# Kernel tuning notes

Hardware: AMD Instinct MI355X
Metric: run time of the kernel (lower is better)

## Reference

```python
import jax, jax.numpy as jnp
import numpy as np

B, T, D, H = 4, 2048, 1024, 16
HD = D // H  # head_dim = 64


def setup_inputs() -> dict:
    key = jax.random.key(0)
    k1, k2, k3 = jax.random.split(key, 3)
    x = jax.random.normal(k1, (B, T, D), dtype=jnp.float32)
    # Linear weights stored [in, out] (transpose of torch's [out, in]); scaled init.
    w_qkv = jax.random.normal(k2, (D, 3 * D), dtype=jnp.float32) / np.sqrt(D)
    b_qkv = jnp.zeros((3 * D,), dtype=jnp.float32)
    w_out = jax.random.normal(k3, (D, D), dtype=jnp.float32) / np.sqrt(D)
    b_out = jnp.zeros((D,), dtype=jnp.float32)
    # Causal mask [1,1,T,T]: 1 where attention allowed (j<=i), 0 elsewhere.
    causal_mask = jnp.tril(jnp.ones((T, T), dtype=jnp.int32))[None, None]
    return {"x": x, "causal_mask": causal_mask, "w_qkv": w_qkv,
            "b_qkv": b_qkv, "w_out": w_out, "b_out": b_out}


def reference(x, causal_mask, w_qkv, b_qkv, w_out, b_out):
    b, t, c = x.shape
    qkv = x @ w_qkv + b_qkv                         # [B,T,3D]
    qkv = qkv.reshape(b, t, 3, H, HD)
    q, k, v = jnp.moveaxis(qkv, 2, 0)               # each [B,T,H,HD]
    q = q.transpose(0, 2, 1, 3)                     # [B,H,T,HD]
    k = k.transpose(0, 2, 1, 3)
    v = v.transpose(0, 2, 1, 3)
    att = jnp.einsum('bhqd,bhkd->bhqk', q, k) / np.sqrt(HD).astype(np.float32)
    att = jnp.where(causal_mask == 0, jnp.float32(-jnp.inf), att)
    att = jax.nn.softmax(att, axis=-1)              # dropout=0.0 (eval)
    y = jnp.einsum('bhqk,bhkd->bhqd', att, v)       # [B,H,T,HD]
    y = y.transpose(0, 2, 1, 3).reshape(b, t, c)    # [B,T,D]
    return y @ w_out + b_out
```

## Files before the change

### kernel.cpp

```cpp
#include <hip/hip_runtime.h>
#include <hip/hip_bf16.h>
#include <stdint.h>

#define BB 4
#define TT 2048
#define DD 1024
#define HH 16
#define HDD 64
#define M1 (BB*TT)
#define N1 (3*DD)
#define KDIM DD

typedef __attribute__((ext_vector_type(8))) short short8;
typedef __attribute__((ext_vector_type(4))) float f32x4;

#if __has_builtin(__builtin_amdgcn_exp2f)
#define EXP2(x) __builtin_amdgcn_exp2f(x)
#else
#define EXP2(x) exp2f(x)
#endif

#define GLOAD_LDS16(gp, lp) \
    __builtin_amdgcn_global_load_lds( \
        (const __attribute__((address_space(1))) void*)(gp), \
        (__attribute__((address_space(3))) void*)(lp), 16, 0, 0)

__device__ __forceinline__ float bf2f(unsigned short u) {
    union { uint32_t u32; float f; } c; c.u32 = ((uint32_t)u) << 16; return c.f;
}
__device__ __forceinline__ unsigned short f2bf(float f) {
    union { float f; uint32_t u32; } c; c.f = f;
    uint32_t u = c.u32;
    return (unsigned short)((u + 0x7FFFu + ((u >> 16) & 1u)) >> 16);
}

template <int CTRL>
__device__ __forceinline__ float dpp_ror(float x) {
    union { float f; int i; } u, r;
    u.f = x;
    r.i = __builtin_amdgcn_update_dpp(u.i, u.i, CTRL, 0xF, 0xF, false);
    return r.f;
}
__device__ __forceinline__ float red_max16(float x) {
    x = fmaxf(x, dpp_ror<0x128>(x));
    x = fmaxf(x, dpp_ror<0x124>(x));
    x = fmaxf(x, dpp_ror<0x122>(x));
    x = fmaxf(x, dpp_ror<0x121>(x));
    return x;
}
__device__ __forceinline__ float red_sum16(float x) {
    x += dpp_ror<0x128>(x);
    x += dpp_ror<0x124>(x);
    x += dpp_ror<0x122>(x);
    x += dpp_ror<0x121>(x);
    return x;
}

__global__ __launch_bounds__(256) void cvt_f32_bf16(
    const float* __restrict__ in, unsigned short* __restrict__ out, int n4)
{
    int i = blockIdx.x * 256 + threadIdx.x;
    if (i >= n4) return;
    float4 v = *(const float4*)&in[(size_t)i * 4];
    ushort4 o;
    o.x = f2bf(v.x); o.y = f2bf(v.y); o.z = f2bf(v.z); o.w = f2bf(v.w);
    *(ushort4*)&out[(size_t)i * 4] = o;
}

__global__ __launch_bounds__(256) void transpose_f32_bf16(
    const float* __restrict__ in, unsigned short* __restrict__ out,
    int R, int C)
{
    __shared__ unsigned short tile[32][33];
    int bx = blockIdx.x;
    int by = blockIdx.y;
    int x = bx*32 + threadIdx.x;
    int y0 = by*32 + threadIdx.y;
    #pragma unroll
    for (int i = 0; i < 32; i += 8)
        tile[threadIdx.y + i][threadIdx.x] = f2bf(in[(size_t)(y0 + i)*C + x]);
    __syncthreads();
    int xo = by*32 + threadIdx.x;
    int yo = bx*32 + threadIdx.y;
    #pragma unroll
    for (int i = 0; i < 32; i += 8)
        out[(size_t)(yo + i)*R + xo] = tile[threadIdx.x][threadIdx.y + i];
}

#define TSTR 132
template <int MODE>
__global__ __launch_bounds__(256) void gemm_bf16_mfma(
    const unsigned short* __restrict__ A, const unsigned short* __restrict__ BT,
    const float* __restrict__ bias, void* __restrict__ Cout, void* __restrict__ Cout2,
    int M, int N, int K)
{
    constexpr int SHSZ = (MODE == 2) ? 128*TSTR : 128*64;
    __shared__ __align__(16) unsigned short Sh[SHSZ];
    unsigned short* As = Sh;
    unsigned short* Bs = Sh + 128*32;
    const int tid  = threadIdx.x;
    const int lane = tid & 63;
    const int wave = tid >> 6;
    const int wm = wave >> 1, wn = wave & 1;
    const int quad = lane >> 4, l16 = lane & 15;
    const int m0 = blockIdx.y * 128, n0 = blockIdx.x * 128;

    f32x4 acc[4][4] = {};

    const int nk = K >> 5;
    for (int kt = 0; kt < nk; ++kt) {
        const int k0 = kt << 5;
        __syncthreads();
        #pragma unroll
        for (int h = 0; h < 2; ++h) {
            int c = tid + h*256;
            int row = c >> 2, seg = c & 3;
            GLOAD_LDS16(&A[(size_t)(m0 + row)*K + k0 + seg*8], &As[row*32 + seg*8]);
            GLOAD_LDS16(&BT[(size_t)(n0 + row)*K + k0 + seg*8], &Bs[row*32 + seg*8]);
        }
        __syncthreads();
        short8 af[4], bf[4];
        #pragma unroll
        for (int mi = 0; mi < 4; ++mi)
            af[mi] = *(short8*)&As[(wm*64 + mi*16 + l16)*32 + quad*8];
        #pragma unroll
        for (int ni = 0; ni < 4; ++ni)
            bf[ni] = *(short8*)&Bs[(wn*64 + ni*16 + l16)*32 + quad*8];
        #pragma unroll
        for (int mi = 0; mi < 4; ++mi)
            #pragma unroll
            for (int ni = 0; ni < 4; ++ni)
                acc[mi][ni] = __builtin_amdgcn_mfma_f32_16x16x32_bf16(
                    af[mi], bf[ni], acc[mi][ni], 0, 0, 0);
    }

    if (MODE == 2 && n0 >= 2048) {
        __syncthreads();
        #pragma unroll
        for (int ni = 0; ni < 4; ++ni) {
            int nl = wn*64 + ni*16 + l16;
            float bv = bias[n0 + nl];
            #pragma unroll
            for (int mi = 0; mi < 4; ++mi) {
                ushort4 pk;
                pk.x = f2bf(acc[mi][ni][0] + bv);
                pk.y = f2bf(acc[mi][ni][1] + bv);
                pk.z = f2bf(acc[mi][ni][2] + bv);
                pk.w = f2bf(acc[mi][ni][3] + bv);
                *(ushort4*)&Sh[nl*TSTR + wm*64 + mi*16 + quad*4] = pk;
            }
        }
        __syncthreads();
        const int bb = m0 >> 11, t0 = m0 & 2047;
        #pragma unroll
        for (int p = 0; p < 8; ++p) {
            int c = tid + p*256;
            int row = c >> 4, ch = c & 15;
            int nv = n0 + row - 2048;
            int hv = nv >> 6, dv = nv & 63;
            *(uint4*)&((unsigned short*)Cout2)[((size_t)((bb*16 + hv)*64 + dv))*2048 + t0 + ch*8] =
                *(uint4*)&Sh[row*TSTR + ch*8];
        }
        return;
    }

    const int cstride = (MODE == 2) ? 2048 : N;
    #pragma unroll
    for (int ni = 0; ni < 4; ++ni) {
        int n = n0 + wn*64 + ni*16 + l16;
        float bv = bias[n];
        #pragma unroll
        for (int mi = 0; mi < 4; ++mi) {
            #pragma unroll
            for (int r = 0; r < 4; ++r) {
                int m = m0 + wm*64 + mi*16 + quad*4 + r;
                float val = acc[mi][ni][r] + bv;
                if (MODE == 1)
                    ((float*)Cout)[(size_t)m*cstride + n] = val;
                else
                    ((unsigned short*)Cout)[(size_t)m*cstride + n] = f2bf(val);
            }
        }
    }
}

#define PST 72
__global__ __launch_bounds__(256, 3) void attn_mfma(
    const unsigned short* __restrict__ QK, const unsigned short* __restrict__ VT,
    unsigned short* __restrict__ Y)
{
    __shared__ __align__(16) unsigned short Sh[16384 + 4*32*PST];

    const int tid  = threadIdx.x;
    const int lane = tid & 63;
    const int wave = tid >> 6;
    const int quad = lane >> 4, l16 = lane & 15;

    const int i = blockIdx.x;
    const int xcd = i & 7, j = i >> 3;
    const int qc = 15 - (j & 15);
    const int bh = xcd + 8*(j >> 4);
    const int b = bh >> 4, h = bh & 15;
    const int q0b = qc * 128;
    const int q0w = q0b + wave*32;
    const size_t qkbase = (size_t)(b*TT) * 2048;
    const size_t vbase  = (size_t)(bh*64) * 2048;
    const int qcol = h*64, kcol = 1024 + h*64;
    const float C2 = 0.18033688011112042f;

    unsigned short* Pw = &Sh[16384 + wave*(32*PST)];

    short8 aq[2][2];
    #pragma unroll
    for (int mt = 0; mt < 2; ++mt)
        #pragma unroll
        for (int kk = 0; kk < 2; ++kk)
            aq[mt][kk] = *(const short8*)&QK[qkbase + (size_t)(q0w + mt*16 + l16)*2048
                                            + qcol + kk*32 + quad*8];

    f32x4 o[2][4] = {};
    float mold[2][4], lsum[2][4];
    #pragma unroll
    for (int mt = 0; mt < 2; ++mt)
        #pragma unroll
        for (int r = 0; r < 4; ++r) { mold[mt][r] = -3.0e38f; lsum[mt][r] = 0.0f; }

    const int nkt = 2*qc + 2;

    auto STAGE = [&](int buf, int kt) {
        const int k0 = kt << 6;
        unsigned short* Kb = &Sh[buf*4096];
        unsigned short* Vb = &Sh[8192 + buf*4096];
        #pragma unroll
        for (int p = 0; p < 2; ++p) {
            int c = p*256 + tid;
            int r = c >> 3;
            int ch = (c & 7) ^ (r & 7);
            GLOAD_LDS16(&QK[qkbase + (size_t)(k0 + r)*2048 + kcol + ch*8], &Kb[c*8]);
        }
        #pragma unroll
        for (int p = 0; p < 2; ++p) {
            int c = p*256 + tid;
            int r = c >> 3;
            int ch = (c & 7) ^ (r & 7);
            GLOAD_LDS16(&VT[vbase + (size_t)r*2048 + k0 + ch*8], &Vb[c*8]);
        }
    };

    STAGE(0, 0);
    asm volatile("s_waitcnt vmcnt(0)" ::: "memory");
    __builtin_amdgcn_s_barrier();

    int cur = 0;
    for (int kt = 0; kt < nkt; ++kt) {
        const int k0 = kt * 64;
        if (kt + 1 < nkt) STAGE(cur ^ 1, kt + 1);

        if (k0 <= q0w + 31) {
            const unsigned short* Kb = &Sh[cur*4096];
            const unsigned short* Vb = &Sh[8192 + cur*4096];

            f32x4 s[2][4];
            #pragma unroll
            for (int nt = 0; nt < 4; ++nt) {
                if (k0 + nt*16 <= q0w + 31) {
                    f32x4 z = {};
                    s[0][nt] = z; s[1][nt] = z;
                    #pragma unroll
                    for (int kk = 0; kk < 2; ++kk) {
                        int r = nt*16 + l16;
                        short8 bk = *(const short8*)&Kb[r*64 + (((kk*4 + quad) ^ (r & 7))*8)];
                        s[0][nt] = __builtin_amdgcn_mfma_f32_16x16x32_bf16(aq[0][kk], bk, s[0][nt], 0, 0, 0);
                        s[1][nt] = __builtin_amdgcn_mfma_f32_16x16x32_bf16(aq[1][kk], bk, s[1][nt], 0, 0, 0);
                    }
                } else {
                    #pragma unroll
                    for (int r = 0; r < 4; ++r) { s[0][nt][r] = -3.0e38f; s[1][nt][r] = -3.0e38f; }
                }
            }

            if (k0 + 63 > q0w) {
                #pragma unroll
                for (int mt = 0; mt < 2; ++mt)
                    #pragma unroll
                    for (int nt = 0; nt < 4; ++nt)
                        #pragma unroll
                        for (int r = 0; r < 4; ++r) {
                            int kg = k0 + nt*16 + l16;
                            int qg = q0w + mt*16 + quad*4 + r;
                            if (kg > qg) s[mt][nt][r] = -3.0e38f;
                        }
            }

            float m2n[2][4], al[2][4];
            #pragma unroll
            for (int mt = 0; mt < 2; ++mt)
                #pragma unroll
                for (int r = 0; r < 4; ++r) {
                    float rm = fmaxf(fmaxf(s[mt][0][r], s[mt][1][r]),
                                     fmaxf(s[mt][2][r], s[mt][3][r]));
                    rm = red_max16(rm);
                    float m2 = fmaxf(mold[mt][r], rm * C2);
                    al[mt][r]  = EXP2(mold[mt][r] - m2);
                    m2n[mt][r] = m2;
                }
            float rs[2][4] = {};
            #pragma unroll
            for (int mt = 0; mt < 2; ++mt)
                #pragma unroll
                for (int nt = 0; nt < 4; ++nt)
                    #pragma unroll
                    for (int r = 0; r < 4; ++r) {
                        float p = EXP2(fmaf(s[mt][nt][r], C2, -m2n[mt][r]));
                        s[mt][nt][r] = p;
                        rs[mt][r] += p;
                    }
            #pragma unroll
            for (int mt = 0; mt < 2; ++mt)
                #pragma unroll
                for (int r = 0; r < 4; ++r) {
                    float t = red_sum16(rs[mt][r]);
                    lsum[mt][r] = lsum[mt][r]*al[mt][r] + t;
                    mold[mt][r] = m2n[mt][r];
                }

            #pragma unroll
            for (int mt = 0; mt < 2; ++mt)
                #pragma unroll
                for (int nt = 0; nt < 4; ++nt)
                    #pragma unroll
                    for (int r = 0; r < 4; ++r) {
                        union { float f; uint32_t u; } c; c.f = s[mt][nt][r];
                        Pw[(mt*16 + quad*4 + r)*PST + nt*16 + l16] =
                            (unsigned short)((c.u + 0x8000u) >> 16);
                    }

            #pragma unroll
            for (int mt = 0; mt < 2; ++mt)
                #pragma unroll
                for (int dt = 0; dt < 4; ++dt)
                    #pragma unroll
                    for (int r = 0; r < 4; ++r)
                        o[mt][dt][r] *= al[mt][r];
            short8 bv[2][4];
            #pragma unroll
            for (int kk = 0; kk < 2; ++kk)
                #pragma unroll
                for (int dt = 0; dt < 4; ++dt) {
                    int r = dt*16 + l16;
                    bv[kk][dt] = *(const short8*)&Vb[r*64 + (((kk*4 + quad) ^ (r & 7))*8)];
                }
            #pragma unroll
            for (int kk = 0; kk < 2; ++kk) {
                short8 ap0 = *(short8*)&Pw[(     l16)*PST + kk*32 + quad*8];
                short8 ap1 = *(short8*)&Pw[(16 + l16)*PST + kk*32 + quad*8];
                #pragma unroll
                for (int dt = 0; dt < 4; ++dt) {
                    o[0][dt] = __builtin_amdgcn_mfma_f32_16x16x32_bf16(ap0, bv[kk][dt], o[0][dt], 0, 0, 0);
                    o[1][dt] = __builtin_amdgcn_mfma_f32_16x16x32_bf16(ap1, bv[kk][dt], o[1][dt], 0, 0, 0);
                }
            }
        }

        asm volatile("s_waitcnt vmcnt(0)" ::: "memory");
        __builtin_amdgcn_s_barrier();
        cur ^= 1;
    }

    #pragma unroll
    for (int mt = 0; mt < 2; ++mt)
        #pragma unroll
        for (int r = 0; r < 4; ++r) {
            float inv = 1.0f / lsum[mt][r];
            int t = q0w + mt*16 + quad*4 + r;
            #pragma unroll
            for (int dt = 0; dt < 4; ++dt)
                Y[((size_t)(b*TT + t))*DD + h*64 + dt*16 + l16] = f2bf(o[mt][dt][r] * inv);
        }
}

extern "C" void kernel_launch(void* const* d_in, const int* in_sizes, int n_in,
                              void* d_out, int out_size, void* d_ws, size_t ws_size,
                              hipStream_t stream)
{
    const float* x    = (const float*)d_in[0];
    const float* wqkv = (const float*)d_in[2];
    const float* bqkv = (const float*)d_in[3];
    const float* wout = (const float*)d_in[4];
    const float* bout = (const float*)d_in[5];
    float* out = (float*)d_out;

    char* ws = (char*)d_ws;
    unsigned short* Xb    = (unsigned short*)ws;
    unsigned short* WqkvT = (unsigned short*)(ws + 16777216);
    unsigned short* WoutT = (unsigned short*)(ws + 23068672);
    unsigned short* QK    = (unsigned short*)(ws + 25165824);
    unsigned short* VTb   = (unsigned short*)(ws + 58720256);
    unsigned short* Ybuf  = (unsigned short*)(ws + 75497472);

    cvt_f32_bf16<<<(M1*KDIM/4 + 255)/256, 256, 0, stream>>>(x, Xb, M1*KDIM/4);
    transpose_f32_bf16<<<dim3(N1/32, KDIM/32), dim3(32, 8), 0, stream>>>(wqkv, WqkvT, KDIM, N1);
    transpose_f32_bf16<<<dim3(DD/32, KDIM/32), dim3(32, 8), 0, stream>>>(wout, WoutT, KDIM, DD);
    gemm_bf16_mfma<2><<<dim3(N1/128, M1/128), 256, 0, stream>>>(Xb, WqkvT, bqkv, QK, VTb, M1, N1, KDIM);
    attn_mfma<<<dim3(1024), 256, 0, stream>>>(QK, VTb, Ybuf);
    gemm_bf16_mfma<1><<<dim3(DD/128, M1/128), 256, 0, stream>>>(Ybuf, WoutT, bout, out, nullptr, M1, DD, KDIM);
}
```

Before: 353.6 us.

## Load V directly to registers, lazy softmax rescale, raise occupancy

The attention kernel stops staging V tiles in LDS and loads them straight from global memory into registers at the start of each key tile, halving shared memory so occupancy can rise from 3 to 4 blocks per CU. It adds a lazy online-softmax rescale: the running max and the O and l rescaling are updated only when some row's new max exceeds the old one by more than 8 (in log2 units), skipping exp work most iterations. It also raises wave priority around the MFMA sections and alternates the q-chunk ordering between block groups to balance causal work. The risks are exposed global-load latency for V, extra register pressure under the tighter launch bound, and bf16 P values up to 2^8 in magnitude before normalisation.

```diff
diff --git a/kernel.cpp b/kernel.cpp
--- a/kernel.cpp
+++ b/kernel.cpp
@@ -185,11 +185,11 @@
 }
 
 #define PST 72
-__global__ __launch_bounds__(256, 3) void attn_mfma(
+__global__ __launch_bounds__(256, 4) void attn_mfma(
     const unsigned short* __restrict__ QK, const unsigned short* __restrict__ VT,
     unsigned short* __restrict__ Y)
 {
-    __shared__ __align__(16) unsigned short Sh[16384 + 4*32*PST];
+    __shared__ __align__(16) unsigned short Sh[8192 + 4*32*PST];
 
     const int tid  = threadIdx.x;
     const int lane = tid & 63;
@@ -198,17 +198,17 @@
 
     const int i = blockIdx.x;
     const int xcd = i & 7, j = i >> 3;
-    const int qc = 15 - (j & 15);
+    const int g = j & 15;
+    const int qc = ((j >> 5) & 1) ? g : 15 - g;
     const int bh = xcd + 8*(j >> 4);
     const int b = bh >> 4, h = bh & 15;
-    const int q0b = qc * 128;
-    const int q0w = q0b + wave*32;
+    const int q0w = qc*128 + wave*32;
     const size_t qkbase = (size_t)(b*TT) * 2048;
     const size_t vbase  = (size_t)(bh*64) * 2048;
     const int qcol = h*64, kcol = 1024 + h*64;
     const float C2 = 0.18033688011112042f;
 
-    unsigned short* Pw = &Sh[16384 + wave*(32*PST)];
+    unsigned short* Pw = &Sh[8192 + wave*(32*PST)];
 
     short8 aq[2][2];
     #pragma unroll
@@ -230,7 +230,6 @@
     auto STAGE = [&](int buf, int kt) {
         const int k0 = kt << 6;
         unsigned short* Kb = &Sh[buf*4096];
-        unsigned short* Vb = &Sh[8192 + buf*4096];
         #pragma unroll
         for (int p = 0; p < 2; ++p) {
             int c = p*256 + tid;
@@ -238,13 +237,6 @@
             int ch = (c & 7) ^ (r & 7);
             GLOAD_LDS16(&QK[qkbase + (size_t)(k0 + r)*2048 + kcol + ch*8], &Kb[c*8]);
         }
-        #pragma unroll
-        for (int p = 0; p < 2; ++p) {
-            int c = p*256 + tid;
-            int r = c >> 3;
-            int ch = (c & 7) ^ (r & 7);
-            GLOAD_LDS16(&VT[vbase + (size_t)r*2048 + k0 + ch*8], &Vb[c*8]);
-        }
     };
 
     STAGE(0, 0);
@@ -258,9 +250,17 @@
 
         if (k0 <= q0w + 31) {
             const unsigned short* Kb = &Sh[cur*4096];
-            const unsigned short* Vb = &Sh[8192 + cur*4096];
+
+            short8 bv[2][4];
+            #pragma unroll
+            for (int kk = 0; kk < 2; ++kk)
+                #pragma unroll
+                for (int dt = 0; dt < 4; ++dt)
+                    bv[kk][dt] = *(const short8*)&VT[vbase + (size_t)(dt*16 + l16)*2048
+                                                     + k0 + kk*32 + quad*8];
 
             f32x4 s[2][4];
+            __builtin_amdgcn_s_setprio(1);
             #pragma unroll
             for (int nt = 0; nt < 4; ++nt) {
                 if (k0 + nt*16 <= q0w + 31) {
@@ -278,6 +278,7 @@
                     for (int r = 0; r < 4; ++r) { s[0][nt][r] = -3.0e38f; s[1][nt][r] = -3.0e38f; }
                 }
             }
+            __builtin_amdgcn_s_setprio(0);
 
             if (k0 + 63 > q0w) {
                 #pragma unroll
@@ -292,18 +293,35 @@
                         }
             }
 
-            float m2n[2][4], al[2][4];
+            float pm[2][4];
             #pragma unroll
             for (int mt = 0; mt < 2; ++mt)
                 #pragma unroll
                 for (int r = 0; r < 4; ++r) {
                     float rm = fmaxf(fmaxf(s[mt][0][r], s[mt][1][r]),
                                      fmaxf(s[mt][2][r], s[mt][3][r]));
-                    rm = red_max16(rm);
-                    float m2 = fmaxf(mold[mt][r], rm * C2);
-                    al[mt][r]  = EXP2(mold[mt][r] - m2);
-                    m2n[mt][r] = m2;
+                    pm[mt][r] = red_max16(rm) * C2;
                 }
+            int need = 0;
+            #pragma unroll
+            for (int mt = 0; mt < 2; ++mt)
+                #pragma unroll
+                for (int r = 0; r < 4; ++r)
+                    need |= (pm[mt][r] > mold[mt][r] + 8.0f);
+            if (__any(need)) {
+                #pragma unroll
+                for (int mt = 0; mt < 2; ++mt)
+                    #pragma unroll
+                    for (int r = 0; r < 4; ++r) {
+                        float m2 = fmaxf(mold[mt][r], pm[mt][r]);
+                        float al = EXP2(mold[mt][r] - m2);
+                        mold[mt][r] = m2;
+                        lsum[mt][r] *= al;
+                        #pragma unroll
+                        for (int dt = 0; dt < 4; ++dt)
+                            o[mt][dt][r] *= al;
+                    }
+            }
             float rs[2][4] = {};
             #pragma unroll
             for (int mt = 0; mt < 2; ++mt)
@@ -311,18 +329,15 @@
                 for (int nt = 0; nt < 4; ++nt)
                     #pragma unroll
                     for (int r = 0; r < 4; ++r) {
-                        float p = EXP2(fmaf(s[mt][nt][r], C2, -m2n[mt][r]));
+                        float p = EXP2(fmaf(s[mt][nt][r], C2, -mold[mt][r]));
                         s[mt][nt][r] = p;
                         rs[mt][r] += p;
                     }
             #pragma unroll
             for (int mt = 0; mt < 2; ++mt)
                 #pragma unroll
-                for (int r = 0; r < 4; ++r) {
-                    float t = red_sum16(rs[mt][r]);
-                    lsum[mt][r] = lsum[mt][r]*al[mt][r] + t;
-                    mold[mt][r] = m2n[mt][r];
-                }
+                for (int r = 0; r < 4; ++r)
+                    lsum[mt][r] += red_sum16(rs[mt][r]);
 
             #pragma unroll
             for (int mt = 0; mt < 2; ++mt)
@@ -335,21 +350,7 @@
                             (unsigned short)((c.u + 0x8000u) >> 16);
                     }
 
-            #pragma unroll
-            for (int mt = 0; mt < 2; ++mt)
-                #pragma unroll
-                for (int dt = 0; dt < 4; ++dt)
-                    #pragma unroll
-                    for (int r = 0; r < 4; ++r)
-                        o[mt][dt][r] *= al[mt][r];
-            short8 bv[2][4];
-            #pragma unroll
-            for (int kk = 0; kk < 2; ++kk)
-                #pragma unroll
-                for (int dt = 0; dt < 4; ++dt) {
-                    int r = dt*16 + l16;
-                    bv[kk][dt] = *(const short8*)&Vb[r*64 + (((kk*4 + quad) ^ (r & 7))*8)];
-                }
+            __builtin_amdgcn_s_setprio(1);
             #pragma unroll
             for (int kk = 0; kk < 2; ++kk) {
                 short8 ap0 = *(short8*)&Pw[(     l16)*PST + kk*32 + quad*8];
@@ -360,6 +361,7 @@
                     o[1][dt] = __builtin_amdgcn_mfma_f32_16x16x32_bf16(ap1, bv[kk][dt], o[1][dt], 0, 0, 0);
                 }
             }
+            __builtin_amdgcn_s_setprio(0);
         }
 
         asm volatile("s_waitcnt vmcnt(0)" ::: "memory");
```

After: 494.3 us. +39.8%, slower.
